# Optimization experiments

Measured on AMD Instinct MI355X. Metric: run time of the kernel, lower is better.

## Reference

```python
import jax, jax.numpy as jnp
import numpy as np

M_CHANNELS = 256
N_KNOTS = 64
EPS = 1e-6


def setup_inputs() -> dict:
    key = jax.random.key(0)
    k_u, k_c = jax.random.split(key)
    u = jax.random.uniform(k_u, (4096, 64, M_CHANNELS), dtype=jnp.float32)
    # knots: per-channel sorted ascending, init linspace(0,1) as in the module
    knots = jnp.tile(jnp.linspace(0.0, 1.0, N_KNOTS, dtype=jnp.float32)[None, :],
                     (M_CHANNELS, 1))
    # coefs init to zeros in the module; use randn for a non-degenerate test
    coefs = jax.random.normal(k_c, (M_CHANNELS, N_KNOTS), dtype=jnp.float32)
    return {"u": u, "knots": knots, "coefs": coefs}


def reference(u, knots, coefs):
    """Piecewise-linear spline eval, vectorized over channels and points.
    u: [..., M], knots/coefs: [M, K] (knots sorted ascending per channel).
    """
    m, K = knots.shape
    orig_shape = u.shape
    flat = u.reshape(-1, m).T  # [M, N]
    # torch.bucketize(right=False) == searchsorted side='left'
    idx = jax.vmap(lambda k, x: jnp.searchsorted(k, x, side='left'))(knots, flat)
    idx0 = jnp.clip(idx - 1, 0, K - 2)  # [M, N]
    idx1 = idx0 + 1
    k0 = jnp.take_along_axis(knots, idx0, axis=1)
    k1 = jnp.take_along_axis(knots, idx1, axis=1)
    c0 = jnp.take_along_axis(coefs, idx0, axis=1)
    c1 = jnp.take_along_axis(coefs, idx1, axis=1)
    t = (flat - k0) / (k1 - k0 + EPS)
    out = c0 + t * (c1 - c0)  # [M, N]
    return out.T.reshape(orig_shape)
```

## Files before the change

kernel.cpp:

```cpp
#include <hip/hip_runtime.h>


#define EPS 1e-6f
#define NCH_GROUP 64
#define STRIDE 65
#define NGROUPS 4
#define BLOCKS_PER_GROUP 256
#define ROWS_PER_TILE 16

__global__ __launch_bounds__(256) void bspline_kernel(
    const float* __restrict__ u, const float* __restrict__ knots,
    const float* __restrict__ coefs, float* __restrict__ out, int n_rows)
{
    __shared__ float sK[NCH_GROUP * STRIDE];
    __shared__ float sC[NCH_GROUP * STRIDE];

    const int t = threadIdx.x;
    const int g = blockIdx.x & (NGROUPS - 1);
    const int b = blockIdx.x >> 2;

    const float* gk = knots + (size_t)g * NCH_GROUP * 64;
    const float* gc = coefs + (size_t)g * NCH_GROUP * 64;
    for (int i = t; i < NCH_GROUP * 64; i += 256) {
        int c = i >> 6;
        int k = i & 63;
        sK[c * STRIDE + k] = gk[i];
        sC[c * STRIDE + k] = gc[i];
    }
    __syncthreads();

    const int col4 = t & 15;
    const int rsub = t >> 4;
    const int lc = col4 * 4;

    float kmin[4], scale[4];
#pragma unroll
    for (int cc = 0; cc < 4; ++cc) {
        float klo = sK[(lc + cc) * STRIDE + 0];
        float khi = sK[(lc + cc) * STRIDE + 63];
        kmin[cc] = klo;
        scale[cc] = 63.0f * __builtin_amdgcn_rcpf(khi - klo);
    }

    const float4* u4 = (const float4*)u;
    float4* o4 = (float4*)out;
    const int colbase = g * 16 + col4;
    const int ntiles = n_rows / ROWS_PER_TILE;

    for (int rt = b; rt < ntiles; rt += BLOCKS_PER_GROUP) {
        int row = rt * ROWS_PER_TILE + rsub;
        size_t idx = (size_t)row * 64 + colbase;
        float4 x4 = u4[idx];
        float4 r;
        const float* xp = &x4.x;
        float* rp = &r.x;
#pragma unroll
        for (int cc = 0; cc < 4; ++cc) {
            float x = xp[cc];
            const float* kp = &sK[(lc + cc) * STRIDE];
            const float* cp = &sC[(lc + cc) * STRIDE];

            float xs = (x - kmin[cc]) * scale[cc];
            int j = (int)xs;
            j = max(0, min(62, j));
            float k0 = kp[j];
            float k1 = kp[j + 1];
            while (j > 0 && k0 >= x) { --j; k1 = k0; k0 = kp[j]; }
            while (j < 62 && k1 < x) { ++j; k0 = k1; k1 = kp[j + 1]; }

            float tt = (x - k0) * __builtin_amdgcn_rcpf(k1 - k0 + EPS);
            float c0 = cp[j];
            float c1 = cp[j + 1];
            rp[cc] = fmaf(tt, c1 - c0, c0);
        }
        o4[idx] = r;
    }
}

extern "C" void kernel_launch(void* const* d_in, const int* in_sizes, int n_in,
                              void* d_out, int out_size, void* d_ws, size_t ws_size,
                              hipStream_t stream) {
    const float* u     = (const float*)d_in[0];
    const float* knots = (const float*)d_in[1];
    const float* coefs = (const float*)d_in[2];
    float* out = (float*)d_out;

    int n_rows = in_sizes[0] / 256;

    dim3 grid(NGROUPS * BLOCKS_PER_GROUP);
    dim3 block(256);
    bspline_kernel<<<grid, block, 0, stream>>>(u, knots, coefs, out, n_rows);
}
```

Measured before the change: 434.3 us.

## Prefetch next tile, use nontemporal loads/stores, halve channel group per block

Splits channels into eight groups of 32 per block, so the shared-memory tables shrink and more blocks can be resident, and raises launch bounds to request occupancy 8. The row loop is restructured to software-prefetch the next tile's input before computing the current one, hiding global load latency. Loads and stores of the streamed input and output use nontemporal builtins to avoid polluting the cache. The risks are higher register pressure from the prefetch and narrower 128-byte row segments per group, which could reduce coalescing efficiency.

```diff
diff --git a/kernel.cpp b/kernel.cpp
--- a/kernel.cpp
+++ b/kernel.cpp
@@ -2,13 +2,15 @@
 
 
 #define EPS 1e-6f
-#define NCH_GROUP 64
+#define NCH_GROUP 32
 #define STRIDE 65
-#define NGROUPS 4
+#define NGROUPS 8
 #define BLOCKS_PER_GROUP 256
-#define ROWS_PER_TILE 16
+#define ROWS_PER_TILE 32
 
-__global__ __launch_bounds__(256) void bspline_kernel(
+typedef float f32x4 __attribute__((ext_vector_type(4)));
+
+__global__ __launch_bounds__(256, 8) void bspline_kernel(
     const float* __restrict__ u, const float* __restrict__ knots,
     const float* __restrict__ coefs, float* __restrict__ out, int n_rows)
 {
@@ -17,7 +19,7 @@
 
     const int t = threadIdx.x;
     const int g = blockIdx.x & (NGROUPS - 1);
-    const int b = blockIdx.x >> 2;
+    const int b = blockIdx.x >> 3;
 
     const float* gk = knots + (size_t)g * NCH_GROUP * 64;
     const float* gc = coefs + (size_t)g * NCH_GROUP * 64;
@@ -29,8 +31,8 @@
     }
     __syncthreads();
 
-    const int col4 = t & 15;
-    const int rsub = t >> 4;
+    const int col4 = t & 7;
+    const int rsub = t >> 3;
     const int lc = col4 * 4;
 
     float kmin[4], scale[4];
@@ -42,21 +44,30 @@
         scale[cc] = 63.0f * __builtin_amdgcn_rcpf(khi - klo);
     }
 
-    const float4* u4 = (const float4*)u;
-    float4* o4 = (float4*)out;
-    const int colbase = g * 16 + col4;
+    const f32x4* u4 = (const f32x4*)u;
+    f32x4* o4 = (f32x4*)out;
+    const int colbase = g * 8 + col4;
     const int ntiles = n_rows / ROWS_PER_TILE;
 
-    for (int rt = b; rt < ntiles; rt += BLOCKS_PER_GROUP) {
-        int row = rt * ROWS_PER_TILE + rsub;
-        size_t idx = (size_t)row * 64 + colbase;
-        float4 x4 = u4[idx];
-        float4 r;
-        const float* xp = &x4.x;
-        float* rp = &r.x;
+    int rt = b;
+    if (rt >= ntiles) return;
+    size_t idx = (size_t)(rt * ROWS_PER_TILE + rsub) * 64 + colbase;
+    f32x4 x4 = __builtin_nontemporal_load(&u4[idx]);
+
+    for (;;) {
+        const int rtn = rt + BLOCKS_PER_GROUP;
+        const bool more = rtn < ntiles;
+        size_t idxn = idx;
+        f32x4 xn = x4;
+        if (more) {
+            idxn = (size_t)(rtn * ROWS_PER_TILE + rsub) * 64 + colbase;
+            xn = __builtin_nontemporal_load(&u4[idxn]);
+        }
+
+        f32x4 r;
 #pragma unroll
         for (int cc = 0; cc < 4; ++cc) {
-            float x = xp[cc];
+            float x = x4[cc];
             const float* kp = &sK[(lc + cc) * STRIDE];
             const float* cp = &sC[(lc + cc) * STRIDE];
 
@@ -71,9 +82,12 @@
             float tt = (x - k0) * __builtin_amdgcn_rcpf(k1 - k0 + EPS);
             float c0 = cp[j];
             float c1 = cp[j + 1];
-            rp[cc] = fmaf(tt, c1 - c0, c0);
+            r[cc] = fmaf(tt, c1 - c0, c0);
         }
-        o4[idx] = r;
+        __builtin_nontemporal_store(r, &o4[idx]);
+
+        if (!more) break;
+        rt = rtn; idx = idxn; x4 = xn;
     }
 }
 
```

New measurement: 443.1 us. 2.0% more time.
